# Performance work log

Measured on AMD Instinct MI355X. Metric: run time of the kernel, lower is better.

## Reference

```python
import jax, jax.numpy as jnp
import numpy as np
from jax import lax

FEATURE_SIZES = (19, 38, 76)   # 608px YOLOv3 grids
NUM_CLASSES = 80
THR_CONF = 0.5
THR_NMS = 0.3
K = 300                        # max detections kept per image (padded, fixed shape)
EPS = 1e-7


def setup_inputs() -> dict:
    key = jax.random.key(0)
    k1, k2 = jax.random.split(key)
    B = 32
    N = sum(f * f * 3 for f in FEATURE_SIZES)  # 22743
    p_yolo = jax.random.normal(k1, (B, N, 5 + NUM_CLASSES), dtype=jnp.float32)
    # normalized anchor xywh table, kept safely inside (0,1)
    ancs = jax.random.uniform(k2, (N, 4), dtype=jnp.float32, minval=0.05, maxval=0.95)
    # fsize_p = np.repeat(feature_sizes, grid^2*3) as in the torch forward
    fs = np.concatenate([np.full((f * f * 3, 2), f, dtype=np.float32) for f in FEATURE_SIZES], axis=0)
    return {"p_yolo": p_yolo, "ancs": ancs, "fsize_p": jnp.asarray(fs)}


def _iou_matrix(b):
    # b: [K,4] ltrb -> [K,K] pairwise IoU
    area = jnp.maximum(b[:, 2] - b[:, 0], 0.0) * jnp.maximum(b[:, 3] - b[:, 1], 0.0)
    lt = jnp.maximum(b[:, None, :2], b[None, :, :2])
    rb = jnp.minimum(b[:, None, 2:], b[None, :, 2:])
    wh = jnp.maximum(rb - lt, 0.0)
    inter = wh[..., 0] * wh[..., 1]
    return inter / (area[:, None] + area[None, :] - inter + EPS)


def _greedy_nms(iou, valid):
    # iou: [K,K] (rows sorted by descending score), valid: [K] bool
    def body(keep, i):
        suppressed = jnp.any((iou[i] > THR_NMS) & keep)
        k_i = valid[i] & jnp.logical_not(suppressed)
        return keep.at[i].set(k_i), k_i
    keep, _ = lax.scan(body, jnp.zeros(valid.shape[0], dtype=bool), jnp.arange(valid.shape[0]))
    return keep


def reference(p_yolo, ancs, fsize_p):
    # sigmoid_(p[:,:,4:])
    conf = jax.nn.sigmoid(p_yolo[..., 4])          # [B,N]
    cls = jax.nn.sigmoid(p_yolo[..., 5:])          # [B,N,C]
    # fix_boxes4yolo3: xy = sigmoid(txy)/fsize + anc_xy ; wh = exp(twh)*anc_wh
    xy = jax.nn.sigmoid(p_yolo[..., :2]) / fsize_p + ancs[..., :2]
    wh = jnp.exp(p_yolo[..., 2:4]) * ancs[..., 2:]
    ltrb = jnp.concatenate([xy - wh * 0.5, xy + wh * 0.5], axis=-1)  # xywh2ltrb, [B,N,4]
    labels = jnp.argmax(cls, axis=-1) + 1                            # [B,N] int

    valid = conf > THR_CONF
    scores_m = jnp.where(valid, conf, 0.0)
    top_scores, idx = lax.top_k(scores_m, K)                         # [B,K], sorted desc
    boxes_k = jnp.take_along_axis(ltrb, idx[..., None], axis=1)      # [B,K,4]
    labels_k = jnp.take_along_axis(labels, idx, axis=1)              # [B,K]
    valid_k = top_scores > THR_CONF

    # label-aware NMS: offset boxes per class (label_nms semantics); coords live in ~[-1,2]
    boxes_off = boxes_k + labels_k.astype(boxes_k.dtype)[..., None] * 4.0
    iou = jax.vmap(_iou_matrix)(boxes_off)                           # [B,K,K]
    keep = jax.vmap(_greedy_nms)(iou, valid_k)                       # [B,K] bool

    B = p_yolo.shape[0]
    ids_batch = jnp.broadcast_to(jnp.arange(B, dtype=jnp.int32)[:, None], (B, K))
    scores_out = top_scores * keep.astype(top_scores.dtype)          # 0 for suppressed/pad
    labels_out = labels_k * keep.astype(labels_k.dtype)
    return ids_batch, boxes_k, labels_out, scores_out
```

## Files before the change

kernel.cpp:

```cpp
#include <hip/hip_runtime.h>
#include <hip/hip_bf16.h>

#pragma clang fp contract(off)

#define BATCH 32
#define NPOS  22743
#define ROW   85
#define KTOP  300
#define KPAD  512
#define CHUNKS 12

#define OFF_IDS    0
#define OFF_BOXES  (BATCH*KTOP)
#define OFF_LABELS (OFF_BOXES + BATCH*KTOP*4)
#define OFF_SCORES (OFF_LABELS + BATCH*KTOP)

#define WS_KEYS   0
#define WS_HIST   (BATCH*NPOS*4)
#define WS_SELIDX (WS_HIST + BATCH*256*4)
#define WS_SELKEY (WS_SELIDX + BATCH*KTOP*4)
#define WS_LABELS (WS_SELKEY + BATCH*KTOP*4)

__device__ __forceinline__ float sigmoidf_ref(float x) {
    return 1.0f / (1.0f + expf(-x));
}

__global__ __launch_bounds__(256) void k_extract(const float* __restrict__ p,
                                                 unsigned* __restrict__ keys,
                                                 unsigned* __restrict__ hist) {
    __shared__ unsigned h[256];
    const int t = threadIdx.x;
    h[t] = 0;
    __syncthreads();
    const int b = blockIdx.x / CHUNKS;
    const int chunk = blockIdx.x % CHUNKS;
    const int base = chunk * 2048;
    for (int it = 0; it < 8; ++it) {
        int n = base + it * 256 + t;
        bool part = (n < NPOS);
        unsigned key = 0, bin = 0;
        if (part) {
            float x = p[((size_t)b * NPOS + n) * ROW + 4];
            float cf = sigmoidf_ref(x);
            key = (cf > 0.5f) ? __float_as_uint(cf) : 0u;
            keys[(size_t)b * NPOS + n] = key;
            bin = key >> 24;
        }
        unsigned long long todo = __ballot(part);
        while (todo) {
            int leader = __ffsll((unsigned long long)todo) - 1;
            unsigned lbin = __shfl(bin, leader);
            unsigned long long same = __ballot(part && (bin == lbin));
            if ((t & 63) == leader) atomicAdd(&h[lbin], (unsigned)__popcll(same));
            todo &= ~same;
        }
    }
    __syncthreads();
    if (h[t]) atomicAdd(&hist[b * 256 + t], h[t]);
}

__global__ __launch_bounds__(256) void k_select(const unsigned* __restrict__ keys,
                                                const unsigned* __restrict__ hist,
                                                int* __restrict__ sel_idx,
                                                unsigned* __restrict__ sel_key) {
    const int b = blockIdx.x;
    const int t = threadIdx.x;
    __shared__ unsigned h[256];
    __shared__ unsigned sc[256];
    __shared__ unsigned bcast_bin, bcast_R;
    __shared__ int cnt, ovf;
    __shared__ unsigned long long arr[KPAD];
    const unsigned* kb = keys + (size_t)b * NPOS;

    unsigned prefix = 0;
    unsigned R = KTOP;

    for (int pass = 0; pass < 4; ++pass) {
        const int shift = 24 - 8 * pass;
        if (pass == 0) {
            h[t] = hist[b * 256 + t];
            __syncthreads();
        } else {
            h[t] = 0;
            __syncthreads();
            for (int n = t; n < NPOS; n += 256) {
                unsigned u = kb[n];
                if ((u >> (shift + 8)) == prefix) atomicAdd(&h[(u >> shift) & 255], 1u);
            }
            __syncthreads();
        }
        sc[t] = h[t];
        __syncthreads();
        for (int off = 1; off < 256; off <<= 1) {
            unsigned add = (t + off < 256) ? sc[t + off] : 0u;
            __syncthreads();
            sc[t] += add;
            __syncthreads();
        }
        unsigned snext = (t < 255) ? sc[t + 1] : 0u;
        if (sc[t] >= R && snext < R) { bcast_bin = (unsigned)t; bcast_R = R - snext; }
        __syncthreads();
        prefix = (prefix << 8) | bcast_bin;
        R = bcast_R;
        __syncthreads();
    }
    const unsigned T = prefix;

    if (t == 0) { cnt = 0; ovf = 0; }
    for (int e = t; e < KPAD; e += 256) arr[e] = 0ull;
    __syncthreads();
    for (int n = t; n < NPOS; n += 256) {
        unsigned u = kb[n];
        if (u >= T) {
            int pos = atomicAdd(&cnt, 1);
            if (pos < KPAD) arr[pos] = ((unsigned long long)u << 32) | (unsigned)(~n);
            else ovf = 1;
        }
    }
    __syncthreads();
    if (ovf) {
        if (t == 0) cnt = 0;
        __syncthreads();
        for (int e = t; e < KPAD; e += 256) arr[e] = 0ull;
        __syncthreads();
        for (int n = t; n < NPOS; n += 256) {
            unsigned u = kb[n];
            if (u > T) {
                int pos = atomicAdd(&cnt, 1);
                arr[pos] = ((unsigned long long)u << 32) | (unsigned)(~n);
            }
        }
        __syncthreads();
        if (t == 0) {
            int c = cnt;
            for (int n = 0; n < NPOS && c < KTOP; ++n)
                if (kb[n] == T) arr[c++] = ((unsigned long long)T << 32) | (unsigned)(~n);
        }
        __syncthreads();
    }
    for (unsigned kk = 2; kk <= KPAD; kk <<= 1)
        for (unsigned j = kk >> 1; j > 0; j >>= 1) {
            __syncthreads();
            for (unsigned e = t; e < KPAD; e += 256) {
                unsigned partner = e ^ j;
                if (partner > e) {
                    bool up = ((e & kk) == 0);
                    unsigned long long a = arr[e], bb = arr[partner];
                    if (up ? (a > bb) : (a < bb)) { arr[e] = bb; arr[partner] = a; }
                }
            }
        }
    __syncthreads();
    for (int e = t; e < KTOP; e += 256) {
        unsigned long long v = arr[KPAD - 1 - e];
        sel_idx[b * KTOP + e] = (int)(~(unsigned)v);
        sel_key[b * KTOP + e] = (unsigned)(v >> 32);
    }
}

__global__ __launch_bounds__(256) void k_decode(const float* __restrict__ p,
                                                const float* __restrict__ ancs,
                                                const float* __restrict__ fsz,
                                                const int* __restrict__ sel_idx,
                                                int* __restrict__ labels,
                                                float* __restrict__ out) {
    const int wid = (int)((blockIdx.x * blockDim.x + threadIdx.x) >> 6);
    const int lane = threadIdx.x & 63;
    if (wid >= BATCH * KTOP) return;
    const int b = wid / KTOP, k = wid % KTOP;
    const int n = sel_idx[b * KTOP + k];
    const size_t base = ((size_t)b * NPOS + n) * ROW;

    float v1 = p[base + lane];
    float v2 = (lane < 21) ? p[base + 64 + lane] : -INFINITY;

    float bv = -INFINITY; int bc = 1 << 20;
    if (lane >= 5) { bv = v1; bc = lane - 5; }
    if (lane < 21) {
        int c2 = 59 + lane;
        if (v2 > bv || (v2 == bv && c2 < bc)) { bv = v2; bc = c2; }
    }
    for (int d = 32; d; d >>= 1) {
        float ov = __shfl_xor(bv, d);
        int   oc = __shfl_xor(bc, d);
        if (ov > bv || (ov == bv && oc < bc)) { bv = ov; bc = oc; }
    }
    const int label = bc + 1;

    float t0 = __shfl(v1, 0), t1 = __shfl(v1, 1), t2 = __shfl(v1, 2), t3 = __shfl(v1, 3);
    if (lane == 0) {
        float f0 = fsz[(size_t)n * 2 + 0], f1 = fsz[(size_t)n * 2 + 1];
        float a0 = ancs[(size_t)n * 4 + 0], a1 = ancs[(size_t)n * 4 + 1];
        float a2 = ancs[(size_t)n * 4 + 2], a3 = ancs[(size_t)n * 4 + 3];
        float cx = sigmoidf_ref(t0) / f0 + a0;
        float cy = sigmoidf_ref(t1) / f1 + a1;
        float w  = expf(t2) * a2;
        float hh = expf(t3) * a3;
        float* ob = out + OFF_BOXES + (size_t)(b * KTOP + k) * 4;
        ob[0] = cx - w * 0.5f;
        ob[1] = cy - hh * 0.5f;
        ob[2] = cx + w * 0.5f;
        ob[3] = cy + hh * 0.5f;
        out[OFF_IDS + b * KTOP + k] = (float)b;
        labels[b * KTOP + k] = label;
    }
}

__global__ __launch_bounds__(256) void k_nms(const float* __restrict__ boxes,
                                             const int* __restrict__ labels,
                                             const unsigned* __restrict__ sel_key,
                                             float* __restrict__ out) {
    const int b = blockIdx.x, t = threadIdx.x;
    __shared__ float bx[KTOP][4];
    __shared__ float area[KTOP];
    __shared__ float score[KTOP];
    __shared__ int   lab[KTOP];
    __shared__ int   validb[KTOP];
    __shared__ unsigned long long O[KTOP * 5];
    __shared__ unsigned long long vb[5];
    __shared__ unsigned long long kw[5];

    for (int k = t; k < KTOP; k += 256) {
        const float* p4 = boxes + (size_t)(b * KTOP + k) * 4;
        int L = labels[b * KTOP + k];
        float off = (float)L * 4.0f;
        float l = p4[0] + off, tp = p4[1] + off, r = p4[2] + off, bt = p4[3] + off;
        bx[k][0] = l; bx[k][1] = tp; bx[k][2] = r; bx[k][3] = bt;
        area[k] = fmaxf(r - l, 0.0f) * fmaxf(bt - tp, 0.0f);
        lab[k] = L;
        unsigned key = sel_key[b * KTOP + k];
        validb[k] = (key > 0x3F000000u) ? 1 : 0;
        score[k] = __uint_as_float(key);
    }
    __syncthreads();

    for (int i = t; i < KTOP; i += 256) {
        float li = bx[i][0], ti = bx[i][1], ri = bx[i][2], bi = bx[i][3], ai = area[i];
        for (int q = 0; q < 5; ++q) {
            unsigned long long wq = 0ull;
            int j0 = q * 64, j1 = min(i, j0 + 64);
            for (int j = j0; j < j1; ++j) {
                float lt0 = fmaxf(li, bx[j][0]);
                float lt1 = fmaxf(ti, bx[j][1]);
                float rb0 = fminf(ri, bx[j][2]);
                float rb1 = fminf(bi, bx[j][3]);
                float ww = fmaxf(rb0 - lt0, 0.0f);
                float hh = fmaxf(rb1 - lt1, 0.0f);
                float inter = ww * hh;
                float iou = inter / (((ai + area[j]) - inter) + 1e-7f);
                if (iou > 0.3f) wq |= 1ull << (j & 63);
            }
            O[i * 5 + q] = wq;
        }
    }
    if (t < 5) {
        unsigned long long v = 0ull;
        for (int j = 0; j < 64; ++j) {
            int idx = t * 64 + j;
            if (idx < KTOP && validb[idx]) v |= 1ull << j;
        }
        vb[t] = v;
    }
    __syncthreads();

    if (t < 64) {
        const int lane = t;
        unsigned long long kwl = 0ull;
        unsigned long long vbl = (lane < 5) ? vb[lane] : 0ull;
        unsigned long long cur = (lane < 5) ? O[lane] : 0ull;
        for (int i = 0; i < KTOP; ++i) {
            unsigned long long nxt = (lane < 5 && i < KTOP - 1) ? O[(i + 1) * 5 + lane] : 0ull;
            bool sup = __any((cur & kwl) != 0ull);
            if (lane == (i >> 6)) {
                bool v = (vbl >> (i & 63)) & 1ull;
                if (v && !sup) kwl |= 1ull << (i & 63);
            }
            cur = nxt;
        }
        if (lane < 5) kw[lane] = kwl;
    }
    __syncthreads();

    for (int k = t; k < KTOP; k += 256) {
        bool kp = (kw[k >> 6] >> (k & 63)) & 1ull;
        out[OFF_SCORES + b * KTOP + k] = kp ? score[k] : 0.0f;
        out[OFF_LABELS + b * KTOP + k] = kp ? (float)lab[k] : 0.0f;
    }
}

extern "C" void kernel_launch(void* const* d_in, const int* in_sizes, int n_in,
                              void* d_out, int out_size, void* d_ws, size_t ws_size,
                              hipStream_t stream) {
    const float* p    = (const float*)d_in[0];
    const float* ancs = (const float*)d_in[1];
    const float* fsz  = (const float*)d_in[2];
    float* out = (float*)d_out;

    char* w = (char*)d_ws;
    unsigned* keys    = (unsigned*)(w + WS_KEYS);
    unsigned* hist    = (unsigned*)(w + WS_HIST);
    int*      sel_idx = (int*)(w + WS_SELIDX);
    unsigned* sel_key = (unsigned*)(w + WS_SELKEY);
    int*      labels  = (int*)(w + WS_LABELS);

    hipMemsetAsync(hist, 0, BATCH * 256 * 4, stream);
    hipLaunchKernelGGL(k_extract, dim3(BATCH * CHUNKS), dim3(256), 0, stream, p, keys, hist);
    hipLaunchKernelGGL(k_select, dim3(BATCH), dim3(256), 0, stream, keys, hist, sel_idx, sel_key);
    hipLaunchKernelGGL(k_decode, dim3((BATCH * KTOP + 3) / 4), dim3(256), 0, stream,
                       p, ancs, fsz, sel_idx, labels, out);
    hipLaunchKernelGGL(k_nms, dim3(BATCH), dim3(256), 0, stream, out + OFF_BOXES, labels, sel_key, out);
}
```

Baseline: 462.3 us.

## Drop fused histogram from extract and use 24-bit keys with three radix passes

Every confidence above 0.5 shares the same top byte, so the extract kernel now stores only the low 24 bits of each valid key. That frees it from building the per-batch histogram, and it becomes a flat one-thread-per-position kernel launched with many more blocks. The select kernel runs three 8-bit radix passes over the keys, all scanning global keys, which is the same number of key scans as before. This removes the hist memset, the ballot/shuffle loop and the global atomics. Scores are rebuilt by OR-ing the exponent byte back in. The overflow fallback also gains bounds checks.

```diff
diff --git a/kernel.cpp b/kernel.cpp
--- a/kernel.cpp
+++ b/kernel.cpp
@@ -8,7 +8,6 @@
 #define ROW   85
 #define KTOP  300
 #define KPAD  512
-#define CHUNKS 12
 
 #define OFF_IDS    0
 #define OFF_BOXES  (BATCH*KTOP)
@@ -16,8 +15,7 @@
 #define OFF_SCORES (OFF_LABELS + BATCH*KTOP)
 
 #define WS_KEYS   0
-#define WS_HIST   (BATCH*NPOS*4)
-#define WS_SELIDX (WS_HIST + BATCH*256*4)
+#define WS_SELIDX (BATCH*NPOS*4)
 #define WS_SELKEY (WS_SELIDX + BATCH*KTOP*4)
 #define WS_LABELS (WS_SELKEY + BATCH*KTOP*4)
 
@@ -26,41 +24,16 @@
 }
 
 __global__ __launch_bounds__(256) void k_extract(const float* __restrict__ p,
-                                                 unsigned* __restrict__ keys,
-                                                 unsigned* __restrict__ hist) {
-    __shared__ unsigned h[256];
-    const int t = threadIdx.x;
-    h[t] = 0;
-    __syncthreads();
-    const int b = blockIdx.x / CHUNKS;
-    const int chunk = blockIdx.x % CHUNKS;
-    const int base = chunk * 2048;
-    for (int it = 0; it < 8; ++it) {
-        int n = base + it * 256 + t;
-        bool part = (n < NPOS);
-        unsigned key = 0, bin = 0;
-        if (part) {
-            float x = p[((size_t)b * NPOS + n) * ROW + 4];
-            float cf = sigmoidf_ref(x);
-            key = (cf > 0.5f) ? __float_as_uint(cf) : 0u;
-            keys[(size_t)b * NPOS + n] = key;
-            bin = key >> 24;
-        }
-        unsigned long long todo = __ballot(part);
-        while (todo) {
-            int leader = __ffsll((unsigned long long)todo) - 1;
-            unsigned lbin = __shfl(bin, leader);
-            unsigned long long same = __ballot(part && (bin == lbin));
-            if ((t & 63) == leader) atomicAdd(&h[lbin], (unsigned)__popcll(same));
-            todo &= ~same;
-        }
-    }
-    __syncthreads();
-    if (h[t]) atomicAdd(&hist[b * 256 + t], h[t]);
+                                                 unsigned* __restrict__ keys) {
+    const int g = blockIdx.x * 256 + threadIdx.x;
+    if (g < BATCH * NPOS) {
+        float x = p[(size_t)g * ROW + 4];
+        float cf = sigmoidf_ref(x);
+        keys[g] = (cf > 0.5f) ? (__float_as_uint(cf) & 0x00FFFFFFu) : 0u;
+    }
 }
 
 __global__ __launch_bounds__(256) void k_select(const unsigned* __restrict__ keys,
-                                                const unsigned* __restrict__ hist,
                                                 int* __restrict__ sel_idx,
                                                 unsigned* __restrict__ sel_key) {
     const int b = blockIdx.x;
@@ -75,20 +48,16 @@
     unsigned prefix = 0;
     unsigned R = KTOP;
 
-    for (int pass = 0; pass < 4; ++pass) {
-        const int shift = 24 - 8 * pass;
-        if (pass == 0) {
-            h[t] = hist[b * 256 + t];
-            __syncthreads();
-        } else {
-            h[t] = 0;
-            __syncthreads();
-            for (int n = t; n < NPOS; n += 256) {
-                unsigned u = kb[n];
-                if ((u >> (shift + 8)) == prefix) atomicAdd(&h[(u >> shift) & 255], 1u);
-            }
-            __syncthreads();
-        }
+    for (int pass = 0; pass < 3; ++pass) {
+        const int shift = 16 - 8 * pass;
+        h[t] = 0;
+        __syncthreads();
+        for (int n = t; n < NPOS; n += 256) {
+            unsigned u = kb[n];
+            if (pass == 0 || (u >> (shift + 8)) == prefix)
+                atomicAdd(&h[(u >> shift) & 255], 1u);
+        }
+        __syncthreads();
         sc[t] = h[t];
         __syncthreads();
         for (int off = 1; off < 256; off <<= 1) {
@@ -127,12 +96,12 @@
             unsigned u = kb[n];
             if (u > T) {
                 int pos = atomicAdd(&cnt, 1);
-                arr[pos] = ((unsigned long long)u << 32) | (unsigned)(~n);
+                if (pos < KPAD) arr[pos] = ((unsigned long long)u << 32) | (unsigned)(~n);
             }
         }
         __syncthreads();
         if (t == 0) {
-            int c = cnt;
+            int c = min(cnt, KPAD - 1);
             for (int n = 0; n < NPOS && c < KTOP; ++n)
                 if (kb[n] == T) arr[c++] = ((unsigned long long)T << 32) | (unsigned)(~n);
         }
@@ -229,8 +198,8 @@
         area[k] = fmaxf(r - l, 0.0f) * fmaxf(bt - tp, 0.0f);
         lab[k] = L;
         unsigned key = sel_key[b * KTOP + k];
-        validb[k] = (key > 0x3F000000u) ? 1 : 0;
-        score[k] = __uint_as_float(key);
+        validb[k] = (key != 0u) ? 1 : 0;
+        score[k] = __uint_as_float(key | 0x3F000000u);
     }
     __syncthreads();
 
@@ -298,14 +267,13 @@
 
     char* w = (char*)d_ws;
     unsigned* keys    = (unsigned*)(w + WS_KEYS);
-    unsigned* hist    = (unsigned*)(w + WS_HIST);
     int*      sel_idx = (int*)(w + WS_SELIDX);
     unsigned* sel_key = (unsigned*)(w + WS_SELKEY);
     int*      labels  = (int*)(w + WS_LABELS);
 
-    hipMemsetAsync(hist, 0, BATCH * 256 * 4, stream);
-    hipLaunchKernelGGL(k_extract, dim3(BATCH * CHUNKS), dim3(256), 0, stream, p, keys, hist);
-    hipLaunchKernelGGL(k_select, dim3(BATCH), dim3(256), 0, stream, keys, hist, sel_idx, sel_key);
+    const int total = BATCH * NPOS;
+    hipLaunchKernelGGL(k_extract, dim3((total + 255) / 256), dim3(256), 0, stream, p, keys);
+    hipLaunchKernelGGL(k_select, dim3(BATCH), dim3(256), 0, stream, keys, sel_idx, sel_key);
     hipLaunchKernelGGL(k_decode, dim3((BATCH * KTOP + 3) / 4), dim3(256), 0, stream,
                        p, ancs, fsz, sel_idx, labels, out);
     hipLaunchKernelGGL(k_nms, dim3(BATCH), dim3(256), 0, stream, out + OFF_BOXES, labels, sel_key, out);
```

After: 453.9 us. Within noise of the previous version (-1.8%).
